# Kernel tuning notes

Measured on AMD Instinct MI355X. Metric: run time of the kernel, lower is better.

The kernel has to match this reference:

```python
import jax, jax.numpy as jnp
import numpy as np

N = 524288   # tokens (accounts)
D = 9        # num_prop_size
E = 2        # expert_size
H = 128      # expert MLP hidden
M = 32       # moe_out
O = 2        # output_size
K = 1        # top-k
LOSS_COF = 0.01
EPS = 1e-10


def setup_inputs() -> dict:
    key = jax.random.key(0)
    ks = jax.random.split(key, 10)
    f32 = jnp.float32
    return {
        "num_prop": jax.random.normal(ks[0], (N, D), f32),
        "cat_prop": jax.random.normal(ks[1], (N, 3), f32),
        "w_gate": jax.random.normal(ks[2], (D, E), f32) * 0.1,
        "W1": jax.random.normal(ks[3], (E, D, H), f32) * 0.1,
        "b1": jax.random.normal(ks[4], (E, H), f32) * 0.01,
        "W2": jax.random.normal(ks[5], (E, H, M), f32) * 0.1,
        "b2": jax.random.normal(ks[6], (E, M), f32) * 0.01,
        "Wout": jax.random.normal(ks[7], (M, O), f32) * 0.1,
        "bout": jax.random.normal(ks[8], (O,), f32) * 0.01,
        "k": K,
    }


def _cv_squared(x):
    # torch: x.var() (unbiased) / (x.mean()**2 + eps)
    return jnp.var(x, ddof=1) / (jnp.mean(x) ** 2 + EPS)


def reference(num_prop, cat_prop, w_gate, W1, b1, W2, b2, Wout, bout, k):
    x = num_prop                                   # eval mode: dropout = identity
    n, e = x.shape[0], w_gate.shape[1]

    # --- top-k gating (eval: clean logits, no noise) ---
    logits = x @ w_gate                            # [N, E]
    top_logits, top_idx = jax.lax.top_k(logits, min(k + 1, e))
    top_k_gates = jax.nn.softmax(top_logits[:, :k], axis=1)   # [N, k]
    rows = jnp.arange(n)[:, None]
    gates = jnp.zeros_like(logits).at[rows, top_idx[:, :k]].set(top_k_gates)  # [N, E]

    importance = gates.sum(axis=0)                 # [E]
    load = (gates > 0).astype(jnp.float32).sum(axis=0)  # [E]
    loss = (_cv_squared(importance) + _cv_squared(load)) * LOSS_COF

    # --- experts: per-expert 2-layer MLP, computed dense (E=2) then gated combine ---
    h = jax.nn.relu(jnp.einsum("nd,edh->neh", x, W1) + b1)    # [N, E, H]
    y_e = jnp.einsum("neh,ehm->nem", h, W2) + b2              # [N, E, M]
    y = jnp.einsum("ne,nem->nm", gates, y_e)                  # [N, M]

    out = y @ Wout + bout                                     # [N, O]
    return (out, loss)
```

## Files before the change

### kernel.cpp

```cpp
#include <hip/hip_runtime.h>

#define NTOK 524288
#define TPB  256
#define TOKB 2048
#define NBLK (NTOK / TOKB)

__device__ __forceinline__ float bf2f(unsigned short u) {
    union { unsigned int i; float f; } v;
    v.i = ((unsigned int)u) << 16;
    return v.f;
}

__device__ __forceinline__ float ldq(const void* p, int i, bool f32) {
    if (f32) return ((const float*)p)[i];
    return bf2f(((const unsigned short*)p)[i]);
}

__global__ void prep_kernel(const void* __restrict__ num_prop,
                            const void* __restrict__ wgate,
                            const void* __restrict__ W1,
                            const void* __restrict__ b1,
                            const void* __restrict__ W2,
                            const void* __restrict__ b2,
                            const void* __restrict__ Wout,
                            const void* __restrict__ bout,
                            unsigned int* __restrict__ cnt1,
                            int* __restrict__ flag,
                            float* __restrict__ bpp,
                            float* __restrict__ wgf,
                            float* __restrict__ wpack)
{
    __shared__ unsigned int bad;
    __shared__ int sflag;
    const int t = threadIdx.x;
    if (t == 0) { bad = 0u; *cnt1 = 0u; }
    __syncthreads();
    if (t < 72) {
        const unsigned short* u = (const unsigned short*)num_prop;
        int e = (u[t] >> 7) & 0xFF;
        if (e < 64 || e > 191) atomicOr(&bad, 1u);
    }
    __syncthreads();
    if (t == 0) { sflag = (int)bad; *flag = (int)bad; }
    __syncthreads();
    const bool f32 = (sflag != 0);

    if (t < 18) wgf[t] = ldq(wgate, t, f32);

    if (t < 4) {
        int e = t >> 1, o = t & 1;
        float acc = ldq(bout, o, f32);
        for (int m = 0; m < 32; ++m)
            acc += ldq(b2, e * 32 + m, f32) * ldq(Wout, m * 2 + o, f32);
        bpp[t] = acc;
    }

    const int e = t >> 7;
    const int j = t & 127;
    float p0 = 0.f, p1 = 0.f;
    for (int m = 0; m < 32; ++m) {
        float w = ldq(W2, (e * 128 + j) * 32 + m, f32);
        p0 += w * ldq(Wout, m * 2 + 0, f32);
        p1 += w * ldq(Wout, m * 2 + 1, f32);
    }
    float* dst = wpack + e * 1536 + j * 12;
    #pragma unroll
    for (int d = 0; d < 9; ++d)
        dst[d] = ldq(W1, (e * 9 + d) * 128 + j, f32);
    dst[9]  = ldq(b1, e * 128 + j, f32);
    dst[10] = p0;
    dst[11] = p1;
}

__global__ __launch_bounds__(TPB, 1)
void moe_main(const void* __restrict__ xg,
              const int* __restrict__ flag,
              const float* __restrict__ wgf,
              const float* __restrict__ bpp,
              const float* __restrict__ wpack,
              unsigned int* __restrict__ cnt1,
              float2* __restrict__ out)
{
    __shared__ __align__(16) float xs[TOKB * 9];
    __shared__ __align__(16) float wsm[3072];
    __shared__ unsigned short smap[TOKB];
    __shared__ unsigned int wcnt[32];

    const int tid  = threadIdx.x;
    const int lane = tid & 63;
    const int wave = tid >> 6;

    const bool f32 = (*flag) != 0;

    #pragma unroll
    for (int i = 0; i < 12; ++i)
        wsm[tid + i * TPB] = wpack[tid + i * TPB];

    if (f32) {
        const float4* xf4 = (const float4*)xg;
        float4* xsv = (float4*)xs;
        const int g4 = blockIdx.x * (TOKB * 9 / 4);
        #pragma unroll
        for (int i = 0; i < 18; ++i)
            xsv[tid + i * TPB] = xf4[g4 + tid + i * TPB];
    } else {
        const unsigned short* xu = (const unsigned short*)xg;
        const int gbase = blockIdx.x * (TOKB * 9);
        for (int i = tid; i < TOKB * 9; i += TPB)
            xs[i] = bf2f(xu[gbase + i]);
    }
    __syncthreads();

    bool e1g[8];
    unsigned long long balg[8];
    #pragma unroll
    for (int g = 0; g < 8; ++g) {
        float l0 = 0.f, l1 = 0.f;
        #pragma unroll
        for (int d = 0; d < 9; ++d) {
            float xv = xs[(g * 256 + tid) * 9 + d];
            l0 = fmaf(xv, wgf[d * 2 + 0], l0);
            l1 = fmaf(xv, wgf[d * 2 + 1], l1);
        }
        e1g[g] = l1 > l0;
        balg[g] = __ballot(e1g[g]);
        if (lane == 0) wcnt[g * 4 + wave] = (unsigned int)__popcll(balg[g]);
    }
    __syncthreads();

    int pres[32]; int run = 0;
    #pragma unroll
    for (int c = 0; c < 32; ++c) { pres[c] = run; run += (int)wcnt[c]; }
    const int n1 = run;
    const int n0 = TOKB - n1;
    const unsigned long long below = (1ull << lane) - 1ull;
    #pragma unroll
    for (int g = 0; g < 8; ++g) {
        const int tok = g * 256 + tid;
        const int pr  = pres[g * 4 + wave] + (int)__popcll(balg[g] & below);
        const int slot = e1g[g] ? (n0 + pr) : (tok - pr);
        smap[slot] = (unsigned short)tok;
    }
    if (tid == 0) atomicAdd(cnt1, (unsigned int)n1);
    __syncthreads();

    const int s0 = tid * 8;
    int tkv[8];
    #pragma unroll
    for (int k = 0; k < 8; ++k) tkv[k] = (int)smap[s0 + k];
    float x[8][9];
    #pragma unroll
    for (int k = 0; k < 8; ++k)
        #pragma unroll
        for (int d = 0; d < 9; ++d) x[k][d] = xs[tkv[k] * 9 + d];

    const int ex = (s0 >= n0) ? 1 : 0;
    const float* wp = wsm + ex * 1536;
    float a0[8], a1[8];
    #pragma unroll
    for (int k = 0; k < 8; ++k) { a0[k] = bpp[ex * 2 + 0]; a1[k] = bpp[ex * 2 + 1]; }

    const float4* q0 = (const float4*)wp;
    float4 A = q0[0], B = q0[1], C = q0[2];
    for (int j = 0; j < 128; ++j) {
        const int jn = (j + 1) & 127;
        const float4* qn = (const float4*)(wp + jn * 12);
        const float4 An = qn[0], Bn = qn[1], Cn = qn[2];
        #pragma unroll
        for (int k = 0; k < 8; ++k) {
            float h = C.y;
            h = fmaf(x[k][0], A.x, h); h = fmaf(x[k][1], A.y, h);
            h = fmaf(x[k][2], A.z, h); h = fmaf(x[k][3], A.w, h);
            h = fmaf(x[k][4], B.x, h); h = fmaf(x[k][5], B.y, h);
            h = fmaf(x[k][6], B.z, h); h = fmaf(x[k][7], B.w, h);
            h = fmaf(x[k][8], C.x, h);
            h = fmaxf(h, 0.f);
            a0[k] = fmaf(h, C.z, a0[k]);
            a1[k] = fmaf(h, C.w, a1[k]);
        }
        A = An; B = Bn; C = Cn;
    }

    const int nw = (n0 & 7) ? (8 - (n0 & 7)) : 0;
    float fx0 = 0.f, fx1 = 0.f; int ftk = 0;
    if (tid < nw) {
        ftk = (int)smap[n0 + tid];
        float xr[9];
        #pragma unroll
        for (int d = 0; d < 9; ++d) xr[d] = xs[ftk * 9 + d];
        fx0 = bpp[2]; fx1 = bpp[3];
        const float* wq = wsm + 1536;
        for (int j = 0; j < 128; ++j) {
            const float4* q = (const float4*)(wq + j * 12);
            const float4 Af = q[0], Bf = q[1], Cf = q[2];
            float h = Cf.y;
            h = fmaf(xr[0], Af.x, h); h = fmaf(xr[1], Af.y, h);
            h = fmaf(xr[2], Af.z, h); h = fmaf(xr[3], Af.w, h);
            h = fmaf(xr[4], Bf.x, h); h = fmaf(xr[5], Bf.y, h);
            h = fmaf(xr[6], Bf.z, h); h = fmaf(xr[7], Bf.w, h);
            h = fmaf(xr[8], Cf.x, h);
            h = fmaxf(h, 0.f);
            fx0 = fmaf(h, Cf.z, fx0);
            fx1 = fmaf(h, Cf.w, fx1);
        }
    }

    __syncthreads();
    float2* ob = (float2*)xs;
    #pragma unroll
    for (int k = 0; k < 8; ++k)
        ob[tkv[k]] = make_float2(a0[k], a1[k]);
    __syncthreads();
    if (tid < nw) ob[ftk] = make_float2(fx0, fx1);
    __syncthreads();
    const int obase = blockIdx.x * TOKB;
    #pragma unroll
    for (int g = 0; g < 8; ++g)
        out[obase + g * 256 + tid] = ob[g * 256 + tid];
}

__global__ void finalize_kernel(const unsigned int* __restrict__ cnt1,
                                float* __restrict__ loss_out)
{
    double c1 = (double)(*cnt1);
    double c0 = (double)NTOK - c1;
    double diff = c0 - c1;
    double mean = (double)NTOK * 0.5;
    double var  = 0.5 * diff * diff;
    double cv2  = var / (mean * mean + 1e-10);
    *loss_out = (float)(0.02 * cv2);
}

extern "C" void kernel_launch(void* const* d_in, const int* in_sizes, int n_in,
                              void* d_out, int out_size, void* d_ws, size_t ws_size,
                              hipStream_t stream) {
    const void* num_prop = d_in[0];
    const void* w_gate   = d_in[2];
    const void* W1       = d_in[3];
    const void* b1       = d_in[4];
    const void* W2       = d_in[5];
    const void* b2       = d_in[6];
    const void* Wout     = d_in[7];
    const void* bout     = d_in[8];

    char* ws = (char*)d_ws;
    unsigned int* cnt1 = (unsigned int*)ws;
    int* flag          = (int*)(ws + 8);
    float* bpp         = (float*)(ws + 16);
    float* wgf         = (float*)(ws + 64);
    float* wpack       = (float*)(ws + 192);

    float*  outf = (float*)d_out;
    float2* out2 = (float2*)d_out;

    hipLaunchKernelGGL(prep_kernel, dim3(1), dim3(256), 0, stream,
                       num_prop, w_gate, W1, b1, W2, b2, Wout, bout,
                       cnt1, flag, bpp, wgf, wpack);
    hipLaunchKernelGGL(moe_main, dim3(NBLK), dim3(TPB), 0, stream,
                       num_prop, flag, wgf, bpp, wpack, cnt1, out2);
    hipLaunchKernelGGL(finalize_kernel, dim3(1), dim3(1), 0, stream,
                       cnt1, outf + (size_t)NTOK * 2);
}
```

Before: 139.9 us.

## Drop shared-memory token staging to raise occupancy, read inputs from global

The 72KB shared buffer that staged each block's token features is removed. Gating and the MLP now read features straight from global memory, with a small float2 output buffer taking its place in shared memory, and launch bounds rise from 1 to 3 blocks per SIMD. The goal is more resident blocks to hide latency and no serialized load-then-compute prologue. In exchange, tokens are re-read from global (cache) with strided 9-float accesses, register pressure is tighter, and the bf16 fallback path is rewritten to compute both experts densely per token.

Result: no change. 139.7 us (-0.1%).

```diff
diff --git a/kernel.cpp b/kernel.cpp
--- a/kernel.cpp
+++ b/kernel.cpp
@@ -72,7 +72,7 @@
     dst[11] = p1;
 }
 
-__global__ __launch_bounds__(TPB, 1)
+__global__ __launch_bounds__(TPB, 3)
 void moe_main(const void* __restrict__ xg,
               const int* __restrict__ flag,
               const float* __restrict__ wgf,
@@ -81,44 +81,71 @@
               unsigned int* __restrict__ cnt1,
               float2* __restrict__ out)
 {
-    __shared__ __align__(16) float xs[TOKB * 9];
     __shared__ __align__(16) float wsm[3072];
     __shared__ unsigned short smap[TOKB];
+    __shared__ float2 ob[TOKB];
     __shared__ unsigned int wcnt[32];
 
     const int tid  = threadIdx.x;
     const int lane = tid & 63;
     const int wave = tid >> 6;
 
-    const bool f32 = (*flag) != 0;
-
     #pragma unroll
     for (int i = 0; i < 12; ++i)
         wsm[tid + i * TPB] = wpack[tid + i * TPB];
-
-    if (f32) {
-        const float4* xf4 = (const float4*)xg;
-        float4* xsv = (float4*)xs;
-        const int g4 = blockIdx.x * (TOKB * 9 / 4);
-        #pragma unroll
-        for (int i = 0; i < 18; ++i)
-            xsv[tid + i * TPB] = xf4[g4 + tid + i * TPB];
-    } else {
+    __syncthreads();
+
+    const bool f32 = (*flag) != 0;
+    const int tbase = blockIdx.x * TOKB;
+
+    if (!f32) {
         const unsigned short* xu = (const unsigned short*)xg;
-        const int gbase = blockIdx.x * (TOKB * 9);
-        for (int i = tid; i < TOKB * 9; i += TPB)
-            xs[i] = bf2f(xu[gbase + i]);
-    }
-    __syncthreads();
+        for (int g = 0; g < 8; ++g) {
+            const int tok = g * 256 + tid;
+            float xr[9];
+            #pragma unroll
+            for (int d = 0; d < 9; ++d)
+                xr[d] = bf2f(xu[(size_t)(tbase + tok) * 9 + d]);
+            float l0 = 0.f, l1 = 0.f;
+            #pragma unroll
+            for (int d = 0; d < 9; ++d) {
+                l0 = fmaf(xr[d], wgf[d * 2 + 0], l0);
+                l1 = fmaf(xr[d], wgf[d * 2 + 1], l1);
+            }
+            const bool e1 = l1 > l0;
+            unsigned long long bal = __ballot(e1);
+            if (lane == 0) atomicAdd(cnt1, (unsigned int)__popcll(bal));
+            float a00 = bpp[0], a01 = bpp[1], a10 = bpp[2], a11 = bpp[3];
+            for (int j = 0; j < 128; ++j) {
+                const float* r0 = wsm + j * 12;
+                const float* r1 = wsm + 1536 + j * 12;
+                float h0 = r0[9], h1 = r1[9];
+                #pragma unroll
+                for (int d = 0; d < 9; ++d) {
+                    h0 = fmaf(xr[d], r0[d], h0);
+                    h1 = fmaf(xr[d], r1[d], h1);
+                }
+                h0 = fmaxf(h0, 0.f); h1 = fmaxf(h1, 0.f);
+                a00 = fmaf(h0, r0[10], a00); a01 = fmaf(h0, r0[11], a01);
+                a10 = fmaf(h1, r1[10], a10); a11 = fmaf(h1, r1[11], a11);
+            }
+            out[tbase + tok] = make_float2(e1 ? a10 : a00, e1 ? a11 : a01);
+        }
+        return;
+    }
+
+    const float* xf = (const float*)xg;
+    const size_t rb = (size_t)tbase * 9;
 
     bool e1g[8];
     unsigned long long balg[8];
     #pragma unroll
     for (int g = 0; g < 8; ++g) {
+        const int tok = g * 256 + tid;
         float l0 = 0.f, l1 = 0.f;
         #pragma unroll
         for (int d = 0; d < 9; ++d) {
-            float xv = xs[(g * 256 + tid) * 9 + d];
+            const float xv = xf[rb + (size_t)tok * 9 + d];
             l0 = fmaf(xv, wgf[d * 2 + 0], l0);
             l1 = fmaf(xv, wgf[d * 2 + 1], l1);
         }
@@ -150,9 +177,11 @@
     for (int k = 0; k < 8; ++k) tkv[k] = (int)smap[s0 + k];
     float x[8][9];
     #pragma unroll
-    for (int k = 0; k < 8; ++k)
-        #pragma unroll
-        for (int d = 0; d < 9; ++d) x[k][d] = xs[tkv[k] * 9 + d];
+    for (int k = 0; k < 8; ++k) {
+        const size_t rk = rb + (size_t)tkv[k] * 9;
+        #pragma unroll
+        for (int d = 0; d < 9; ++d) x[k][d] = xf[rk + d];
+    }
 
     const int ex = (s0 >= n0) ? 1 : 0;
     const float* wp = wsm + ex * 1536;
@@ -186,8 +215,9 @@
     if (tid < nw) {
         ftk = (int)smap[n0 + tid];
         float xr[9];
-        #pragma unroll
-        for (int d = 0; d < 9; ++d) xr[d] = xs[ftk * 9 + d];
+        const size_t rk = rb + (size_t)ftk * 9;
+        #pragma unroll
+        for (int d = 0; d < 9; ++d) xr[d] = xf[rk + d];
         fx0 = bpp[2]; fx1 = bpp[3];
         const float* wq = wsm + 1536;
         for (int j = 0; j < 128; ++j) {
@@ -205,18 +235,15 @@
         }
     }
 
-    __syncthreads();
-    float2* ob = (float2*)xs;
     #pragma unroll
     for (int k = 0; k < 8; ++k)
         ob[tkv[k]] = make_float2(a0[k], a1[k]);
     __syncthreads();
     if (tid < nw) ob[ftk] = make_float2(fx0, fx1);
     __syncthreads();
-    const int obase = blockIdx.x * TOKB;
     #pragma unroll
     for (int g = 0; g < 8; ++g)
-        out[obase + g * 256 + tid] = ob[g * 256 + tid];
+        out[tbase + g * 256 + tid] = ob[g * 256 + tid];
 }
 
 __global__ void finalize_kernel(const unsigned int* __restrict__ cnt1,
```
